# Kernel tuning notes

Hardware: AMD Instinct MI355X
Metric: run time of the kernel (lower is better)

The kernel has to match this reference:

```python
import jax, jax.numpy as jnp
import numpy as np

N_NODES = 50000
N_EDGES = 1600000
IN_DIM = 128
OUT_DIM = 128
NEG_SLOPE = 0.01  # torch F.leaky_relu default


def setup_inputs() -> dict:
    key = jax.random.key(0)
    ks = jax.random.split(key, 8)
    feat = jax.random.normal(ks[0], (N_NODES, IN_DIM), dtype=jnp.float32)
    src = jax.random.randint(ks[1], (N_EDGES,), 0, N_NODES, dtype=jnp.int32)
    dst = jax.random.randint(ks[2], (N_EDGES,), 0, N_NODES, dtype=jnp.int32)
    W = jax.random.normal(ks[3], (IN_DIM, OUT_DIM), dtype=jnp.float32) / np.sqrt(IN_DIM)
    b = jax.random.normal(ks[4], (OUT_DIM,), dtype=jnp.float32) * 0.01
    attn_w = jax.random.normal(ks[5], (2 * OUT_DIM, 1), dtype=jnp.float32) / np.sqrt(2 * OUT_DIM)
    attn_b = jax.random.normal(ks[6], (1,), dtype=jnp.float32) * 0.01
    mask_weights = jnp.ones((IN_DIM,), dtype=jnp.float32)
    return {"feat": feat, "src": src, "dst": dst, "W": W, "b": b,
            "attn_w": attn_w, "attn_b": attn_b, "mask_weights": mask_weights}


def reference(feat, src, dst, W, b, attn_w, attn_b, mask_weights):
    N = feat.shape[0]
    d = W.shape[1]
    # feature masking + linear projection: [N, out_dim]
    h = (feat * jax.nn.sigmoid(mask_weights)) @ W + b
    # edge scores: attn_mlp(cat([h_src, h_dst])) split into two GEMVs to avoid
    # materializing the [E, 2d] concat
    s_src = (h @ attn_w[:d]).squeeze(-1)   # [N]
    s_dst = (h @ attn_w[d:]).squeeze(-1)   # [N]
    score = s_src[src] + s_dst[dst] + attn_b[0]          # [E]
    score = jnp.where(score >= 0, score, NEG_SLOPE * score)  # leaky_relu
    # segment softmax grouped by destination node (dgl.softmax over in-edges)
    mx = jax.ops.segment_max(score, dst, num_segments=N)     # [N]
    mx = jnp.where(jnp.isfinite(mx), mx, 0.0)                 # nodes w/o edges
    ex = jnp.exp(score - mx[dst])                             # [E]
    denom = jax.ops.segment_sum(ex, dst, num_segments=N)     # [N]
    a = ex / jnp.where(denom == 0, 1.0, denom)[dst]           # [E]
    # weighted scatter-sum: h_new[v] = sum_{(u,v) in E} a_uv * h[u]
    h_new = jax.ops.segment_sum(h[src] * a[:, None], dst, num_segments=N)
    return h_new
```

## Files before the change

### kernel.cpp

```cpp
#include <hip/hip_runtime.h>
#include <hip/hip_fp16.h>
#include <math.h>

#define N_NODES 50000
#define N_EDGES 1600000
#define NB 2000
#define NPB 25
#define NCH 100
#define EPC 16000
#define CAPC 32
#define CAP_LDS 1280
#define SPLIT 8
#define BPS (NB / SPLIT)
#define PLACE_BLOCKS (NCH * SPLIT)
#define PROJ_BLOCKS ((N_NODES + 31) / 32)
#define NBG 5
#define NGRP (NBG * NPB)
#define GQ_BLOCKS ((NB / (NBG * 2)) * 8)

typedef _Float16 f16x8 __attribute__((ext_vector_type(8)));
typedef float f32x4 __attribute__((ext_vector_type(4)));


__global__ __launch_bounds__(256) void k_prep(const float* __restrict__ W,
                                              const float* __restrict__ b,
                                              const float* __restrict__ attn_w,
                                              __half* __restrict__ w16q,
                                              float* __restrict__ waSD,
                                              float* __restrict__ cst) {
    const int blk = blockIdx.x, t = threadIdx.x;
    if (blk < 8) {
        const int k = blk * 16 + (t >> 4), sub = t & 15;
        const float4* W4 = (const float4*)W;
        float4 w0 = W4[k * 32 + sub * 2];
        float4 w1 = W4[k * 32 + sub * 2 + 1];
        const int j0 = sub * 8;
        float pS = w0.x * attn_w[j0]     + w0.y * attn_w[j0 + 1]
                 + w0.z * attn_w[j0 + 2] + w0.w * attn_w[j0 + 3]
                 + w1.x * attn_w[j0 + 4] + w1.y * attn_w[j0 + 5]
                 + w1.z * attn_w[j0 + 6] + w1.w * attn_w[j0 + 7];
        float pD = w0.x * attn_w[128 + j0]     + w0.y * attn_w[128 + j0 + 1]
                 + w0.z * attn_w[128 + j0 + 2] + w0.w * attn_w[128 + j0 + 3]
                 + w1.x * attn_w[128 + j0 + 4] + w1.y * attn_w[128 + j0 + 5]
                 + w1.z * attn_w[128 + j0 + 6] + w1.w * attn_w[128 + j0 + 7];
        pS += __shfl_down(pS, 8); pS += __shfl_down(pS, 4);
        pS += __shfl_down(pS, 2); pS += __shfl_down(pS, 1);
        pD += __shfl_down(pD, 8); pD += __shfl_down(pD, 4);
        pD += __shfl_down(pD, 2); pD += __shfl_down(pD, 1);
        if (sub == 0) { waSD[k] = pS; waSD[128 + k] = pD; }
    } else if (blk < 40) {
        for (int e = (blk - 8) * 256 + t; e < 16384; e += 8192) {
            int j = e & 7, l = (e >> 3) & 63, kb = (e >> 9) & 3, ct = e >> 11;
            int k = kb * 32 + (l >> 4) * 8 + j;
            int c = ct * 16 + (l & 15);
            w16q[e] = __float2half(W[k * 128 + c]);
        }
    } else if (t < 64) {
        float vS = b[t] * attn_w[t]       + b[t + 64] * attn_w[t + 64];
        float vD = b[t] * attn_w[128 + t] + b[t + 64] * attn_w[192 + t];
        for (int off = 32; off; off >>= 1) {
            vS += __shfl_down(vS, off);
            vD += __shfl_down(vD, off);
        }
        if (t == 0) { cst[0] = vS; cst[1] = vD; }
    }
}

__global__ __launch_bounds__(512) void k_fusedA(const float* __restrict__ feat,
                                                const float* __restrict__ b,
                                                const float* __restrict__ mask,
                                                const int* __restrict__ src,
                                                const int* __restrict__ dst,
                                                __half* __restrict__ h16q,
                                                float* __restrict__ s_src,
                                                float* __restrict__ s_dst,
                                                int* __restrict__ cnt,
                                                unsigned* __restrict__ gep,
                                                const __half* __restrict__ w16q,
                                                const float* __restrict__ waSD,
                                                const float* __restrict__ cst) {
    __shared__ __align__(16) char smem[33024];
    const int blk = blockIdx.x;
    const int t = threadIdx.x;

    if (blk < PLACE_BLOCKS) {
        int* cur = (int*)smem;
        unsigned* lcell = (unsigned*)(smem + 1024);
        const int c = blk >> 3, sp = blk & 7;
        const int b0 = sp * BPS;
        for (int i = t; i < BPS; i += 512) cur[i] = 0;
        __syncthreads();
        const int q0 = c * (EPC / 4);
        for (int q = t; q < EPC / 4; q += 512) {
            int4 s4 = ((const int4*)src)[q0 + q];
            int4 d4 = ((const int4*)dst)[q0 + q];
            int ss[4] = {s4.x, s4.y, s4.z, s4.w};
            int dd[4] = {d4.x, d4.y, d4.z, d4.w};
#pragma unroll
            for (int k = 0; k < 4; k++) {
                int d = dd[k];
                int bkt = d / NPB;
                if (bkt >= b0 && bkt < b0 + BPS) {
                    int dl = d - bkt * NPB;
                    int lb = bkt - b0;
                    int r = atomicAdd(&cur[lb], 1);
                    if (r < CAPC)
                        lcell[lb * CAPC + r] = ((unsigned)ss[k] << 5) | (unsigned)dl;
                }
            }
        }
        __syncthreads();
        const uint4* lc4 = (const uint4*)lcell;
        uint4* gp4 = (uint4*)gep;
        for (int idx = t; idx < BPS * (CAPC / 4); idx += 512) {
            int i = idx >> 3, q = idx & 7;
            gp4[((size_t)(b0 + i) * NCH + c) * 8 + q] = lc4[idx];
        }
        for (int i = t; i < BPS; i += 512) cnt[c * NB + b0 + i] = min(cur[i], CAPC);
    } else {
        float* sAW = (float*)(smem + 8192);
        float* sAD = (float*)(smem + 8704);
        float* sig = (float*)(smem + 9216);
        const int bb = blk - PLACE_BLOCKS;
        const int row0 = bb * 32;
        if (t < 128) {
            sig[t] = 1.f / (1.f + expf(-mask[t]));
            sAW[t] = waSD[t];
            sAD[t] = waSD[128 + t];
        }
        __syncthreads();
        for (int idx = t; idx < 32 * 32; idx += 512) {
            int r = idx >> 5, c4 = idx & 31;
            int grow = row0 + r;
            float4 f;
            if (grow < N_NODES) f = ((const float4*)feat)[grow * 32 + c4];
            else f = make_float4(0.f, 0.f, 0.f, 0.f);
            int c = c4 * 4;
            ushort4 pk;
            pk.x = __half_as_ushort(__float2half(f.x * sig[c]));
            pk.y = __half_as_ushort(__float2half(f.y * sig[c + 1]));
            pk.z = __half_as_ushort(__float2half(f.z * sig[c + 2]));
            pk.w = __half_as_ushort(__float2half(f.w * sig[c + 3]));
            int byte = (r * 256 + c4 * 8) ^ ((r & 7) << 4);
            *(ushort4*)(smem + byte) = pk;
        }
        __syncthreads();
        const int wv = t >> 6, l = t & 63;
        const int lr = l & 15, lk = l >> 4;
        const f16x8* wq = (const f16x8*)w16q;
        f32x4 acc0 = {0.f, 0.f, 0.f, 0.f};
        f32x4 acc1 = {0.f, 0.f, 0.f, 0.f};
#pragma unroll
        for (int kb = 0; kb < 4; kb++) {
            f16x8 Bf = wq[(wv * 4 + kb) * 64 + l];
            int co = kb * 64 + lk * 16;
            f16x8 A0 = *(const f16x8*)(smem + ((lr * 256 + co) ^ ((lr & 7) << 4)));
            f16x8 A1 = *(const f16x8*)(smem + (((16 + lr) * 256 + co) ^ ((lr & 7) << 4)));
            acc0 = __builtin_amdgcn_mfma_f32_16x16x32_f16(A0, Bf, acc0, 0, 0, 0);
            acc1 = __builtin_amdgcn_mfma_f32_16x16x32_f16(A1, Bf, acc1, 0, 0, 0);
        }
        {
            const int r2 = t >> 4, sub = t & 15;
            f16x8 xv = *(const f16x8*)(smem + ((r2 * 256 + sub * 16) ^ ((r2 & 7) << 4)));
            float ss = 0.f, sd = 0.f;
#pragma unroll
            for (int q = 0; q < 8; q++) {
                float v = (float)xv[q];
                int jj = sub * 8 + q;
                ss = fmaf(v, sAW[jj], ss);
                sd = fmaf(v, sAD[jj], sd);
            }
            ss += __shfl_down(ss, 8); ss += __shfl_down(ss, 4);
            ss += __shfl_down(ss, 2); ss += __shfl_down(ss, 1);
            sd += __shfl_down(sd, 8); sd += __shfl_down(sd, 4);
            sd += __shfl_down(sd, 2); sd += __shfl_down(sd, 1);
            int grow = row0 + r2;
            if (sub == 0 && grow < N_NODES) {
                s_src[grow] = ss + cst[0];
                s_dst[grow] = sd + cst[1];
            }
        }
        const float bj = b[wv * 16 + lr];
        __half* hp = h16q + (size_t)(wv >> 1) * (N_NODES * 32) + ((wv & 1) * 16 + lr);
#pragma unroll
        for (int reg = 0; reg < 4; reg++) {
            int n0 = row0 + lk * 4 + reg;
            if (n0 < N_NODES) hp[(size_t)n0 * 32] = __float2half(acc0[reg] + bj);
            int n1 = n0 + 16;
            if (n1 < N_NODES) hp[(size_t)n1 * 32] = __float2half(acc1[reg] + bj);
        }
    }
}

__global__ __launch_bounds__(256) void k_sort(const float* __restrict__ s_src,
                                              const float* __restrict__ s_dst,
                                              const float* __restrict__ attn_b,
                                              const int* __restrict__ cnt,
                                              unsigned* gep,
                                              int* __restrict__ rp_g) {
    __shared__ unsigned raw[CAP_LDS];
    __shared__ unsigned srt[CAP_LDS];
    __shared__ float wbuf[CAP_LDS];
    __shared__ int ccnt[NCH];
    __shared__ int coff[NCH];
    __shared__ int hist[NPB];
    __shared__ int rp[NPB + 1];
    __shared__ int curn[NPB];
    __shared__ float sdl[NPB];
    __shared__ float dsum[NPB];
    __shared__ float dinv[NPB];
    __shared__ int totsh;
    const int bkt = blockIdx.x;
    const int t = threadIdx.x;
    if (t < NCH) ccnt[t] = cnt[t * NB + bkt];
    if (t < NPB) { hist[t] = 0; dsum[t] = 0.f; sdl[t] = s_dst[bkt * NPB + t]; }
    __syncthreads();
    if (t < 64) {
        int i0 = 2 * t, i1 = 2 * t + 1;
        int a0 = (i0 < NCH) ? ccnt[i0] : 0;
        int a1 = (i1 < NCH) ? ccnt[i1] : 0;
        int s = a0 + a1, incl = s;
#pragma unroll
        for (int off = 1; off < 64; off <<= 1) {
            int v = __shfl_up(incl, off);
            if (t >= off) incl += v;
        }
        int excl = incl - s;
        if (i0 < NCH) coff[i0] = excl;
        if (i1 < NCH) coff[i1] = excl + a0;
        if (t == 63) totsh = incl;
    }
    __syncthreads();
    int total = totsh;
    if (total > CAP_LDS) total = CAP_LDS;
    unsigned* gb = gep + (size_t)bkt * (NCH * CAPC);
    for (int i = t; i < NCH * CAPC; i += 256) {
        unsigned e = gb[i];
        int cell = i >> 5, slot = i & 31;
        if (slot < ccnt[cell]) {
            int pos = coff[cell] + slot;
            if (pos < CAP_LDS) {
                raw[pos] = e;
                atomicAdd(&hist[e & 31], 1);
            }
        }
    }
    __syncthreads();
    if (t == 0) {
        int run = 0;
        for (int j = 0; j < NPB; j++) { rp[j] = run; curn[j] = run; run += hist[j]; }
        rp[NPB] = run;
    }
    __syncthreads();
    const float ab = attn_b[0];
    for (int i = t; i < total; i += 256) {
        unsigned e = raw[i];
        int dl = e & 31;
        int s = (int)(e >> 5);
        float sc = s_src[s] + sdl[dl] + ab;
        sc = sc >= 0.f ? sc : 0.01f * sc;
        float w = expf(sc);
        int pos = atomicAdd(&curn[dl], 1);
        srt[pos] = ((unsigned)s << 16) | (unsigned)dl;
        wbuf[pos] = w;
        atomicAdd(&dsum[dl], w);
    }
    __syncthreads();
    if (t < NPB) dinv[t] = dsum[t] > 0.f ? 1.f / dsum[t] : 0.f;
    __syncthreads();
    for (int i = t; i < total; i += 256) {
        unsigned e = srt[i];
        float a = wbuf[i] * dinv[e & 31];
        gb[i] = (e & 0xFFFF0000u) | (unsigned)__half_as_ushort(__float2half(a));
    }
    if (t <= NPB) rp_g[bkt * 32 + t] = rp[t];
}

__device__ __forceinline__ void accum8(float4& A, float4& B, uint4 u, float w) {
    __half2 p0 = *(const __half2*)&u.x;
    __half2 p1 = *(const __half2*)&u.y;
    __half2 p2 = *(const __half2*)&u.z;
    __half2 p3 = *(const __half2*)&u.w;
    float2 f0 = __half22float2(p0), f1 = __half22float2(p1);
    float2 f2 = __half22float2(p2), f3 = __half22float2(p3);
    A.x = fmaf(w, f0.x, A.x); A.y = fmaf(w, f0.y, A.y);
    A.z = fmaf(w, f1.x, A.z); A.w = fmaf(w, f1.y, A.w);
    B.x = fmaf(w, f2.x, B.x); B.y = fmaf(w, f2.y, B.y);
    B.z = fmaf(w, f3.x, B.z); B.w = fmaf(w, f3.y, B.w);
}

__device__ __forceinline__ float wdec(unsigned e) {
    return __half2float(__ushort_as_half((unsigned short)(e & 0xFFFFu)));
}

__global__ __launch_bounds__(512) void k_gather(const __half* __restrict__ h16q,
                                                const unsigned* __restrict__ gep,
                                                const int* __restrict__ rp_g,
                                                float* __restrict__ out) {
    __shared__ unsigned se[NBG * CAP_LDS];
    __shared__ int rp[NBG * 32];
    const int blk = blockIdx.x;
    const int x = blk & 7;
    const int qq = x & 3;
    const int bg = ((blk >> 3) << 1) + (x >> 2);
    const int bkt0 = bg * NBG;
    const int t = threadIdx.x;
    if (t < NBG * 32 && (t & 31) <= NPB)
        rp[t] = rp_g[(bkt0 + (t >> 5)) * 32 + (t & 31)];
    __syncthreads();
#pragma unroll
    for (int b = 0; b < NBG; b++) {
        const unsigned* gb = gep + (size_t)(bkt0 + b) * (NCH * CAPC);
        const int tot = rp[b * 32 + NPB];
        for (int i = t; i < tot; i += 512) se[b * CAP_LDS + i] = gb[i];
    }
    __syncthreads();
    const int g = t >> 2, dp = t & 3;
    if (g < NGRP) {
        const int b = g / NPB, n = g - b * NPB;
        const int lo = rp[b * 32 + n], hi = rp[b * 32 + n + 1];
        const unsigned* seb = se + b * CAP_LDS;
        const uint4* hq = (const uint4*)h16q + (size_t)qq * (N_NODES * 4) + dp;
        float4 A = {0.f, 0.f, 0.f, 0.f}, B = {0.f, 0.f, 0.f, 0.f};
        for (int i = lo; i < hi; i += 4) {
            unsigned e0 = seb[i];
            unsigned e1 = (i + 1 < hi) ? seb[i + 1] : 0u;
            unsigned e2 = (i + 2 < hi) ? seb[i + 2] : 0u;
            unsigned e3 = (i + 3 < hi) ? seb[i + 3] : 0u;
            uint4 u0 = hq[(e0 >> 16) * 4];
            uint4 u1 = hq[(e1 >> 16) * 4];
            uint4 u2 = hq[(e2 >> 16) * 4];
            uint4 u3 = hq[(e3 >> 16) * 4];
            accum8(A, B, u0, wdec(e0));
            accum8(A, B, u1, wdec(e1));
            accum8(A, B, u2, wdec(e2));
            accum8(A, B, u3, wdec(e3));
        }
        float4* o = (float4*)(out + (size_t)(bg * 125 + g) * 128 + qq * 32 + dp * 8);
        o[0] = A;
        o[1] = B;
    }
}

extern "C" void kernel_launch(void* const* d_in, const int* in_sizes, int n_in,
                              void* d_out, int out_size, void* d_ws, size_t ws_size,
                              hipStream_t stream) {
    const float* feat   = (const float*)d_in[0];
    const int*   src    = (const int*)d_in[1];
    const int*   dst    = (const int*)d_in[2];
    const float* W      = (const float*)d_in[3];
    const float* b      = (const float*)d_in[4];
    const float* attn_w = (const float*)d_in[5];
    const float* attn_b = (const float*)d_in[6];
    const float* mask   = (const float*)d_in[7];
    float* out = (float*)d_out;

    char* ws = (char*)d_ws;
    __half*   h16q  = (__half*)(ws + 0);
    float*    s_src = (float*)(ws + 12800000);
    float*    s_dst = (float*)(ws + 13000000);
    int*      cnt   = (int*)(ws + 13200000);
    unsigned* gep   = (unsigned*)(ws + 14000000);
    int*      rp_g  = (int*)(ws + 39600000);
    __half*   w16q  = (__half*)(ws + 39856000);
    float*    waSD  = (float*)(ws + 39888768);
    float*    cst   = (float*)(ws + 39889792);

    k_prep<<<41, 256, 0, stream>>>(W, b, attn_w, w16q, waSD, cst);
    k_fusedA<<<PLACE_BLOCKS + PROJ_BLOCKS, 512, 0, stream>>>(
        feat, b, mask, src, dst, h16q, s_src, s_dst, cnt, gep, w16q, waSD, cst);
    k_sort<<<NB, 256, 0, stream>>>(s_src, s_dst, attn_b, cnt, gep, rp_g);
    k_gather<<<GQ_BLOCKS, 512, 0, stream>>>(h16q, gep, rp_g, out);
}
```

Measured before the change: 176.5 us.

## Pad per-node edge segments to multiples of eight for vectorized gather loads

The softmax kernel now pads each destination node's edge range to a multiple of eight and fills the padding with zero-weight entries. This lets the gather kernel read edge descriptors as uint4 pairs and issue eight feature loads per iteration with no bounds checks. It also transposes the count array so each bucket reads contiguous counts, unrolls the score computation to prefetch s_src values, and switches to __expf. The trade-offs are lower staging capacity (CAP_STG) to make room for the padding, extra gathers of row 0 for padded slots, and slightly less accurate exponentials.

```diff
diff --git a/kernel.cpp b/kernel.cpp
--- a/kernel.cpp
+++ b/kernel.cpp
@@ -10,6 +10,7 @@
 #define EPC 16000
 #define CAPC 32
 #define CAP_LDS 1280
+#define CAP_STG 1080
 #define SPLIT 8
 #define BPS (NB / SPLIT)
 #define PLACE_BLOCKS (NCH * SPLIT)
@@ -116,7 +117,8 @@
             int i = idx >> 3, q = idx & 7;
             gp4[((size_t)(b0 + i) * NCH + c) * 8 + q] = lc4[idx];
         }
-        for (int i = t; i < BPS; i += 512) cnt[c * NB + b0 + i] = min(cur[i], CAPC);
+        for (int i = t; i < BPS; i += 512)
+            cnt[(b0 + i) * NCH + c] = min(cur[i], CAPC);
     } else {
         float* sAW = (float*)(smem + 8192);
         float* sAD = (float*)(smem + 8704);
@@ -212,7 +214,7 @@
     __shared__ int totsh;
     const int bkt = blockIdx.x;
     const int t = threadIdx.x;
-    if (t < NCH) ccnt[t] = cnt[t * NB + bkt];
+    if (t < NCH) ccnt[t] = cnt[bkt * NCH + t];
     if (t < NPB) { hist[t] = 0; dsum[t] = 0.f; sdl[t] = s_dst[bkt * NPB + t]; }
     __syncthreads();
     if (t < 64) {
@@ -232,14 +234,14 @@
     }
     __syncthreads();
     int total = totsh;
-    if (total > CAP_LDS) total = CAP_LDS;
+    if (total > CAP_STG) total = CAP_STG;
     unsigned* gb = gep + (size_t)bkt * (NCH * CAPC);
     for (int i = t; i < NCH * CAPC; i += 256) {
         unsigned e = gb[i];
         int cell = i >> 5, slot = i & 31;
         if (slot < ccnt[cell]) {
             int pos = coff[cell] + slot;
-            if (pos < CAP_LDS) {
+            if (pos < CAP_STG) {
                 raw[pos] = e;
                 atomicAdd(&hist[e & 31], 1);
             }
@@ -248,27 +250,47 @@
     __syncthreads();
     if (t == 0) {
         int run = 0;
-        for (int j = 0; j < NPB; j++) { rp[j] = run; curn[j] = run; run += hist[j]; }
+        for (int j = 0; j < NPB; j++) {
+            rp[j] = run; curn[j] = run;
+            run += (hist[j] + 7) & ~7;
+        }
         rp[NPB] = run;
     }
     __syncthreads();
+    const int totp = rp[NPB];
+    for (int i = t; i < totp; i += 256) { srt[i] = 0u; wbuf[i] = 0.f; }
+    __syncthreads();
     const float ab = attn_b[0];
-    for (int i = t; i < total; i += 256) {
-        unsigned e = raw[i];
-        int dl = e & 31;
-        int s = (int)(e >> 5);
-        float sc = s_src[s] + sdl[dl] + ab;
-        sc = sc >= 0.f ? sc : 0.01f * sc;
-        float w = expf(sc);
-        int pos = atomicAdd(&curn[dl], 1);
-        srt[pos] = ((unsigned)s << 16) | (unsigned)dl;
-        wbuf[pos] = w;
-        atomicAdd(&dsum[dl], w);
+    {
+        unsigned ev[5];
+        float ssv[5];
+#pragma unroll
+        for (int k = 0; k < 5; k++) {
+            int i = t + k * 256;
+            ev[k] = (i < total) ? raw[i] : 0xFFFFFFFFu;
+        }
+#pragma unroll
+        for (int k = 0; k < 5; k++)
+            ssv[k] = s_src[(ev[k] != 0xFFFFFFFFu) ? (int)(ev[k] >> 5) : 0];
+#pragma unroll
+        for (int k = 0; k < 5; k++) {
+            if (ev[k] != 0xFFFFFFFFu) {
+                unsigned e = ev[k];
+                int dl = e & 31;
+                float sc = ssv[k] + sdl[dl] + ab;
+                sc = sc >= 0.f ? sc : 0.01f * sc;
+                float w = __expf(sc);
+                int pos = atomicAdd(&curn[dl], 1);
+                srt[pos] = ((e >> 5) << 16) | (unsigned)dl;
+                wbuf[pos] = w;
+                atomicAdd(&dsum[dl], w);
+            }
+        }
     }
     __syncthreads();
     if (t < NPB) dinv[t] = dsum[t] > 0.f ? 1.f / dsum[t] : 0.f;
     __syncthreads();
-    for (int i = t; i < total; i += 256) {
+    for (int i = t; i < totp; i += 256) {
         unsigned e = srt[i];
         float a = wbuf[i] * dinv[e & 31];
         gb[i] = (e & 0xFFFF0000u) | (unsigned)__half_as_ushort(__float2half(a));
@@ -276,7 +298,8 @@
     if (t <= NPB) rp_g[bkt * 32 + t] = rp[t];
 }
 
-__device__ __forceinline__ void accum8(float4& A, float4& B, uint4 u, float w) {
+__device__ __forceinline__ void accum8(float4& A, float4& B, uint4 u, unsigned e) {
+    float w = __half2float(__ushort_as_half((unsigned short)(e & 0xFFFFu)));
     __half2 p0 = *(const __half2*)&u.x;
     __half2 p1 = *(const __half2*)&u.y;
     __half2 p2 = *(const __half2*)&u.z;
@@ -287,10 +310,6 @@
     A.z = fmaf(w, f1.x, A.z); A.w = fmaf(w, f1.y, A.w);
     B.x = fmaf(w, f2.x, B.x); B.y = fmaf(w, f2.y, B.y);
     B.z = fmaf(w, f3.x, B.z); B.w = fmaf(w, f3.y, B.w);
-}
-
-__device__ __forceinline__ float wdec(unsigned e) {
-    return __half2float(__ushort_as_half((unsigned short)(e & 0xFFFFu)));
 }
 
 __global__ __launch_bounds__(512) void k_gather(const __half* __restrict__ h16q,
@@ -319,22 +338,28 @@
     if (g < NGRP) {
         const int b = g / NPB, n = g - b * NPB;
         const int lo = rp[b * 32 + n], hi = rp[b * 32 + n + 1];
-        const unsigned* seb = se + b * CAP_LDS;
+        const uint4* se4 = (const uint4*)(se + b * CAP_LDS);
         const uint4* hq = (const uint4*)h16q + (size_t)qq * (N_NODES * 4) + dp;
         float4 A = {0.f, 0.f, 0.f, 0.f}, B = {0.f, 0.f, 0.f, 0.f};
-        for (int i = lo; i < hi; i += 4) {
-            unsigned e0 = seb[i];
-            unsigned e1 = (i + 1 < hi) ? seb[i + 1] : 0u;
-            unsigned e2 = (i + 2 < hi) ? seb[i + 2] : 0u;
-            unsigned e3 = (i + 3 < hi) ? seb[i + 3] : 0u;
-            uint4 u0 = hq[(e0 >> 16) * 4];
-            uint4 u1 = hq[(e1 >> 16) * 4];
-            uint4 u2 = hq[(e2 >> 16) * 4];
-            uint4 u3 = hq[(e3 >> 16) * 4];
-            accum8(A, B, u0, wdec(e0));
-            accum8(A, B, u1, wdec(e1));
-            accum8(A, B, u2, wdec(e2));
-            accum8(A, B, u3, wdec(e3));
+        for (int i = lo; i < hi; i += 8) {
+            uint4 ea = se4[i >> 2];
+            uint4 eb = se4[(i >> 2) + 1];
+            uint4 u0 = hq[(ea.x >> 16) * 4];
+            uint4 u1 = hq[(ea.y >> 16) * 4];
+            uint4 u2 = hq[(ea.z >> 16) * 4];
+            uint4 u3 = hq[(ea.w >> 16) * 4];
+            uint4 u4 = hq[(eb.x >> 16) * 4];
+            uint4 u5 = hq[(eb.y >> 16) * 4];
+            uint4 u6 = hq[(eb.z >> 16) * 4];
+            uint4 u7 = hq[(eb.w >> 16) * 4];
+            accum8(A, B, u0, ea.x);
+            accum8(A, B, u1, ea.y);
+            accum8(A, B, u2, ea.z);
+            accum8(A, B, u3, ea.w);
+            accum8(A, B, u4, eb.x);
+            accum8(A, B, u5, eb.y);
+            accum8(A, B, u6, eb.z);
+            accum8(A, B, u7, eb.w);
         }
         float4* o = (float4*)(out + (size_t)(bg * 125 + g) * 128 + qq * 32 + dp * 8);
         o[0] = A;
```

Result: slower. 180.5 us (+2.2%).
